# Performance work log

Hardware: AMD Instinct MI355X
Metric: run time of the kernel (lower is better)

The kernel has to match this reference:

```python
import jax, jax.numpy as jnp
import numpy as np

H = 8
D = 64  # head_dim = node_dim // num_heads = 512 // 8
NODE = 512
EPS = 1e-5


def setup_inputs() -> dict:
    key = jax.random.key(0)
    ks = jax.random.split(key, 8)
    S, IN = 4096, 1024
    return {
        "protT5_emb": jax.random.normal(ks[0], (S, IN), jnp.float32),
        "contact_matrix": jax.random.uniform(ks[1], (S, S), jnp.float32),
        "Wq": jax.random.normal(ks[2], (NODE, IN), jnp.float32) * 0.02,
        "bq": jnp.zeros((NODE,), jnp.float32),
        "Wk": jax.random.normal(ks[3], (NODE, IN), jnp.float32) * 0.02,
        "bk": jnp.zeros((NODE,), jnp.float32),
        "Wv": jax.random.normal(ks[4], (NODE, IN), jnp.float32) * 0.02,
        "bv": jnp.zeros((NODE,), jnp.float32),
        "Wc": jnp.ones((1, H, 1, 1), jnp.float32),
        "Wo": jax.random.normal(ks[5], (NODE, NODE), jnp.float32) * 0.02,
        "bo": jnp.zeros((NODE,), jnp.float32),
        "gamma": jnp.ones((NODE,), jnp.float32),
        "beta": jnp.zeros((NODE,), jnp.float32),
    }


def reference(protT5_emb, contact_matrix, Wq, bq, Wk, bk, Wv, bv, Wc, Wo, bo, gamma, beta):
    S = protT5_emb.shape[0]
    # QKV projections -> [H, S, D]
    Q = (protT5_emb @ Wq.T + bq).reshape(S, H, D).transpose(1, 0, 2)
    K = (protT5_emb @ Wk.T + bk).reshape(S, H, D).transpose(1, 0, 2)
    V = (protT5_emb @ Wv.T + bv).reshape(S, H, D).transpose(1, 0, 2)
    # raw scores [H, S, S]
    attn_raw = jnp.einsum('hsd,htd->hst', Q, K) / jnp.sqrt(jnp.float32(D))
    # multiplicative contact mask, per-head learnable scale
    contact_mask = contact_matrix[None, :, :] * Wc.reshape(H, 1, 1)
    attn_weight = jax.nn.softmax(attn_raw * contact_mask, axis=-1)
    attn_output = jnp.einsum('hst,htd->hsd', attn_weight, V)  # [H, S, D]
    # FAITHFUL to torch: transpose(0,1).view(S,-1) on [1,H,S,D] flattens in
    # (head, seq, dim) order -> scrambled [S, H*D] reshape, not head concat.
    attn_output = attn_output.reshape(S, H * D)
    aug = attn_output @ Wo.T + bo
    x = aug + protT5_emb[:, :NODE]
    mu = jnp.mean(x, axis=-1, keepdims=True)
    var = jnp.mean((x - mu) ** 2, axis=-1, keepdims=True)
    return (x - mu) * jax.lax.rsqrt(var + EPS) * gamma + beta
```

## Files before the change

kernel.cpp:

```cpp
#include <hip/hip_runtime.h>
#include <stdint.h>

#define SEQ 4096
#define INDIM 1024
#define NODEDIM 512
#define NH 8
#define HD 64
#define LSTR 72

typedef __bf16 bf16x8 __attribute__((ext_vector_type(8)));
typedef float f32x4 __attribute__((ext_vector_type(4)));

#define GLOAD_LDS(gp, lp) \
    __builtin_amdgcn_global_load_lds( \
        (const __attribute__((address_space(1))) void*)(gp), \
        (__attribute__((address_space(3))) void*)(lp), 16, 0, 0)

__device__ __forceinline__ unsigned short f2bf(float f) {
    union { float f; uint32_t u; } v; v.f = f;
    uint32_t u = v.u;
    uint32_t r = (u + 0x7fffu + ((u >> 16) & 1u)) >> 16;
    return (unsigned short)r;
}

__device__ __forceinline__ float fast_exp2(float x) {
    float r;
    asm volatile("v_exp_f32 %0, %1" : "=v"(r) : "v"(x));
    return r;
}

__global__ __launch_bounds__(256) void cvt_all(const float* __restrict__ emb,
                                               const float* __restrict__ Wq,
                                               const float* __restrict__ Wk,
                                               const float* __restrict__ Wv,
                                               const float* __restrict__ Wo,
                                               unsigned short* __restrict__ demb,
                                               unsigned short* __restrict__ dwqkv,
                                               unsigned short* __restrict__ dwo) {
    int b = blockIdx.x;
    const float* src;
    unsigned short* dst;
    int off;
    if (b < 4096)      { src = emb; dst = demb;            off = b; }
    else if (b < 4608) { src = Wq;  dst = dwqkv;           off = b - 4096; }
    else if (b < 5120) { src = Wk;  dst = dwqkv + 524288;  off = b - 4608; }
    else if (b < 5632) { src = Wv;  dst = dwqkv + 1048576; off = b - 5120; }
    else               { src = Wo;  dst = dwo;             off = b - 5632; }
    int i = (off * 256 + threadIdx.x) * 4;
    float4 v = *(const float4*)(src + i);
    ushort4 o;
    o.x = f2bf(v.x); o.y = f2bf(v.y); o.z = f2bf(v.z); o.w = f2bf(v.w);
    *(ushort4*)(dst + i) = o;
}

__global__ __launch_bounds__(256) void qkv_gemm(const unsigned short* __restrict__ A,
                                                const unsigned short* __restrict__ B,
                                                const float* __restrict__ bq,
                                                const float* __restrict__ bk,
                                                const float* __restrict__ bv,
                                                unsigned short* __restrict__ Qo,
                                                unsigned short* __restrict__ Ko,
                                                unsigned short* __restrict__ VTo) {
    __shared__ unsigned short As[128 * 32];
    __shared__ unsigned short Bs[128 * 32];
    __shared__ unsigned short Ts[128 * 40];
    const int tid = threadIdx.x;
    const int lane = tid & 63, wave = tid >> 6;
    const int wm = wave >> 1, wn = wave & 1;
    const int quad = lane >> 4, l16 = lane & 15;
    const int m0 = blockIdx.x * 128;
    const int n0 = blockIdx.y * 128;

    const int srow = tid >> 2, sqq = tid & 3;

    f32x4 acc[4][4] = {};

    for (int k0 = 0; k0 < INDIM; k0 += 32) {
        __syncthreads();
        for (int i = 0; i < 2; ++i) {
            int row = srow + 64 * i;
            GLOAD_LDS(A + (size_t)(m0 + row) * INDIM + k0 + sqq * 8, &As[row * 32 + sqq * 8]);
            GLOAD_LDS(B + (size_t)(n0 + row) * INDIM + k0 + sqq * 8, &Bs[row * 32 + sqq * 8]);
        }
        __syncthreads();
        bf16x8 af[4], bf[4];
        for (int mi = 0; mi < 4; ++mi)
            af[mi] = *(const bf16x8*)&As[(wm * 64 + mi * 16 + l16) * 32 + quad * 8];
        for (int ni = 0; ni < 4; ++ni)
            bf[ni] = *(const bf16x8*)&Bs[(wn * 64 + ni * 16 + l16) * 32 + quad * 8];
        for (int mi = 0; mi < 4; ++mi)
            for (int ni = 0; ni < 4; ++ni)
                acc[mi][ni] = __builtin_amdgcn_mfma_f32_16x16x32_bf16(af[mi], bf[ni], acc[mi][ni], 0, 0, 0);
    }

    if (blockIdx.y < 8) {
        unsigned short* outp = (blockIdx.y < 4) ? Qo : Ko;
        const float* biasp = (blockIdx.y < 4) ? bq : bk;
        for (int mi = 0; mi < 4; ++mi)
            for (int ni = 0; ni < 4; ++ni)
                for (int r = 0; r < 4; ++r) {
                    int s = m0 + wm * 64 + mi * 16 + quad * 4 + r;
                    int n = n0 + wn * 64 + ni * 16 + l16;
                    int h = (n >> 6) & 7;
                    int dd = n & 63;
                    float v = acc[mi][ni][r] + biasp[n & 511];
                    outp[((size_t)h * SEQ + s) * HD + dd] = f2bf(v);
                }
    } else {
        for (int chunk = 0; chunk < 4; ++chunk) {
            const int cwm = chunk >> 1;
            const int milo = (chunk & 1) * 2;
            __syncthreads();
            if (wm == cwm) {
                for (int mi2 = 0; mi2 < 2; ++mi2) {
                    int mi = milo + mi2;
                    for (int ni = 0; ni < 4; ++ni) {
                        int ddf = wn * 64 + ni * 16 + l16;
                        float bias = bv[(n0 + ddf) & 511];
                        for (int r = 0; r < 4; ++r) {
                            int sl = mi2 * 16 + quad * 4 + r;
                            Ts[ddf * 40 + sl] = f2bf(acc[mi][ni][r] + bias);
                        }
                    }
                }
            }
            __syncthreads();
            for (int pass = 0; pass < 2; ++pass) {
                int c = pass * 256 + tid;
                int row = c >> 2, part = c & 3;
                int nfull = n0 + row;
                int h = (nfull >> 6) & 7, dd = nfull & 63;
                *(bf16x8*)(VTo + ((size_t)h * HD + dd) * SEQ + m0 + chunk * 32 + part * 8) =
                    *(const bf16x8*)&Ts[row * 40 + part * 8];
            }
        }
    }
}

__global__ __launch_bounds__(256, 3) void attn_kernel(const unsigned short* __restrict__ Q,
                                                      const unsigned short* __restrict__ K,
                                                      const unsigned short* __restrict__ VT,
                                                      const float* __restrict__ CM,
                                                      const float* __restrict__ Wc,
                                                      float* __restrict__ O0,
                                                      float* __restrict__ O1,
                                                      float* __restrict__ O2,
                                                      float* __restrict__ O3,
                                                      float* __restrict__ l0,
                                                      float* __restrict__ l1,
                                                      float* __restrict__ l2,
                                                      float* __restrict__ l3,
                                                      int nsplit) {
    __shared__ unsigned short QPs[128 * LSTR];
    __shared__ unsigned short Ks[64 * LSTR];
    __shared__ unsigned short Vs[64 * LSTR];
    const int tid = threadIdx.x;
    const int lane = tid & 63, wave = tid >> 6;
    const int quad = lane >> 4, l16 = lane & 15;
    const int h = blockIdx.y;
    const int q0 = blockIdx.x * 128;
    const int split = blockIdx.z;
    float* __restrict__ Op = (split == 0) ? O0 : (split == 1) ? O1 : (split == 2) ? O2 : O3;
    float* __restrict__ lp = (split == 0) ? l0 : (split == 1) ? l1 : (split == 2) ? l2 : l3;
    const float wch = Wc[h] * 0.125f * 1.44269504f;

    const int qt = 64 / nsplit, rt = 64 % nsplit;
    const int tb_tiles = split * qt + (split < rt ? split : rt);
    const int ntiles = qt + (split < rt ? 1 : 0);
    const int tbeg = tb_tiles * 64;
    const int tend = tbeg + ntiles * 64;

    for (int i = 0; i < 4; ++i) {
        int c = tid + 256 * i;
        int row = c >> 3, part = c & 7;
        bf16x8 v = *(const bf16x8*)(Q + ((size_t)h * SEQ + q0 + row) * HD + part * 8);
        for (int j = 0; j < 8; ++j) v[j] = (__bf16)((float)v[j] * wch);
        *(bf16x8*)&QPs[row * LSTR + part * 8] = v;
    }

    const int srow0 = tid >> 3, spart = tid & 7;
    const int srow1 = (tid + 256) >> 3;
    const unsigned short* kp0 = K + ((size_t)h * SEQ + tbeg + srow0) * HD + spart * 8;
    const unsigned short* kp1 = K + ((size_t)h * SEQ + tbeg + srow1) * HD + spart * 8;
    const unsigned short* vp0 = VT + ((size_t)h * HD + srow0) * SEQ + tbeg + spart * 8;
    const unsigned short* vp1 = VT + ((size_t)h * HD + srow1) * SEQ + tbeg + spart * 8;
    bf16x8 kr0 = *(const bf16x8*)kp0;
    bf16x8 kr1 = *(const bf16x8*)kp1;
    bf16x8 vr0 = *(const bf16x8*)vp0;
    bf16x8 vr1 = *(const bf16x8*)vp1;

    __syncthreads();
    bf16x8 a[2][2];
    for (int mi = 0; mi < 2; ++mi) {
        a[mi][0] = *(const bf16x8*)&QPs[(wave * 32 + mi * 16 + l16) * LSTR + quad * 8];
        a[mi][1] = *(const bf16x8*)&QPs[(wave * 32 + mi * 16 + l16) * LSTR + 32 + quad * 8];
    }

    f32x4 O[2][4] = {};
    float l_part[2][4] = {};
    const float* cmbase0 = CM + (size_t)(q0 + wave * 32 + quad * 4) * SEQ + l16;
    const float* cmbase1 = cmbase0 + (size_t)16 * SEQ;
    const int sw = (l16 >> 2) & 3;

    for (int t0 = tbeg; t0 < tend; t0 += 64) {
        float cmv[2][4][4];
        for (int r = 0; r < 4; ++r)
            for (int nt = 0; nt < 4; ++nt) {
                cmv[0][r][nt] = cmbase0[(size_t)r * SEQ + t0 + nt * 16];
                cmv[1][r][nt] = cmbase1[(size_t)r * SEQ + t0 + nt * 16];
            }

        __syncthreads();
        *(bf16x8*)&Ks[srow0 * LSTR + spart * 8] = kr0;
        *(bf16x8*)&Ks[srow1 * LSTR + spart * 8] = kr1;
        *(bf16x8*)&Vs[srow0 * LSTR + spart * 8] = vr0;
        *(bf16x8*)&Vs[srow1 * LSTR + spart * 8] = vr1;
        __syncthreads();

        if (t0 + 64 < tend) {
            kr0 = *(const bf16x8*)(kp0 + (size_t)(t0 + 64 - tbeg) * HD);
            kr1 = *(const bf16x8*)(kp1 + (size_t)(t0 + 64 - tbeg) * HD);
            vr0 = *(const bf16x8*)(vp0 + (t0 + 64 - tbeg));
            vr1 = *(const bf16x8*)(vp1 + (t0 + 64 - tbeg));
        }

        f32x4 sc[2][4];
        for (int nt = 0; nt < 4; ++nt) {
            bf16x8 b0 = *(const bf16x8*)&Ks[(nt * 16 + l16) * LSTR + quad * 8];
            bf16x8 b1 = *(const bf16x8*)&Ks[(nt * 16 + l16) * LSTR + 32 + quad * 8];
            for (int mi = 0; mi < 2; ++mi) {
                f32x4 z = {0.f, 0.f, 0.f, 0.f};
                z = __builtin_amdgcn_mfma_f32_16x16x32_bf16(a[mi][0], b0, z, 0, 0, 0);
                z = __builtin_amdgcn_mfma_f32_16x16x32_bf16(a[mi][1], b1, z, 0, 0, 0);
                sc[mi][nt] = z;
            }
        }

        for (int mi = 0; mi < 2; ++mi)
            for (int r = 0; r < 4; ++r)
                for (int nt = 0; nt < 4; ++nt) {
                    float pv = fast_exp2(sc[mi][nt][r] * cmv[mi][r][nt]);
                    l_part[mi][r] += pv;
                    union { float f; uint32_t u; } pu; pu.f = pv;
                    QPs[(wave * 32 + mi * 16 + quad * 4 + r) * LSTR
                        + (((nt * 2 + (l16 >> 3)) ^ quad) << 3) + (l16 & 7)] =
                        (unsigned short)(pu.u >> 16);
                }

        asm volatile("s_waitcnt lgkmcnt(0)" ::: "memory");

        bf16x8 pa[2][2];
        for (int mi = 0; mi < 2; ++mi) {
            pa[mi][0] = *(const bf16x8*)&QPs[(wave * 32 + mi * 16 + l16) * LSTR + ((quad ^ sw) << 3)];
            pa[mi][1] = *(const bf16x8*)&QPs[(wave * 32 + mi * 16 + l16) * LSTR + 32 + ((quad ^ sw) << 3)];
        }
        for (int nt = 0; nt < 4; ++nt) {
            bf16x8 vb0 = *(const bf16x8*)&Vs[(nt * 16 + l16) * LSTR + quad * 8];
            bf16x8 vb1 = *(const bf16x8*)&Vs[(nt * 16 + l16) * LSTR + 32 + quad * 8];
            for (int mi = 0; mi < 2; ++mi) {
                f32x4 o = O[mi][nt];
                o = __builtin_amdgcn_mfma_f32_16x16x32_bf16(pa[mi][0], vb0, o, 0, 0, 0);
                o = __builtin_amdgcn_mfma_f32_16x16x32_bf16(pa[mi][1], vb1, o, 0, 0, 0);
                O[mi][nt] = o;
            }
        }
    }

    for (int mi = 0; mi < 2; ++mi)
        for (int r = 0; r < 4; ++r) {
            float s = l_part[mi][r];
            for (int off = 1; off < 16; off <<= 1) s += __shfl_xor(s, off);
            l_part[mi][r] = s;
        }
    if (l16 == 0)
        for (int mi = 0; mi < 2; ++mi)
            for (int r = 0; r < 4; ++r)
                lp[(size_t)h * SEQ + q0 + wave * 32 + mi * 16 + quad * 4 + r] = l_part[mi][r];
    for (int mi = 0; mi < 2; ++mi)
        for (int nt = 0; nt < 4; ++nt)
            for (int r = 0; r < 4; ++r) {
                int sg = q0 + wave * 32 + mi * 16 + quad * 4 + r;
                Op[((size_t)h * SEQ + sg) * HD + nt * 16 + l16] = O[mi][nt][r];
            }
}

__global__ __launch_bounds__(256) void combine_kernel(const float* __restrict__ O0,
                                                      const float* __restrict__ O1,
                                                      const float* __restrict__ O2,
                                                      const float* __restrict__ O3,
                                                      const float* __restrict__ l0,
                                                      const float* __restrict__ l1,
                                                      const float* __restrict__ l2,
                                                      const float* __restrict__ l3,
                                                      int nsplit,
                                                      unsigned short* __restrict__ AO) {
    int idx = blockIdx.x * 256 + threadIdx.x;
    int e = idx * 4;
    int row = e >> 6;
    float4 a = *(const float4*)(O0 + e);
    float4 b = *(const float4*)(O1 + e);
    float x = a.x + b.x, y = a.y + b.y, z = a.z + b.z, w = a.w + b.w;
    float ls = l0[row] + l1[row];
    if (nsplit >= 3) {
        float4 c = *(const float4*)(O2 + e);
        x += c.x; y += c.y; z += c.z; w += c.w;
        ls += l2[row];
    }
    if (nsplit >= 4) {
        float4 d = *(const float4*)(O3 + e);
        x += d.x; y += d.y; z += d.z; w += d.w;
        ls += l3[row];
    }
    float linv = 1.f / ls;
    ushort4 o;
    o.x = f2bf(x * linv);
    o.y = f2bf(y * linv);
    o.z = f2bf(z * linv);
    o.w = f2bf(w * linv);
    *(ushort4*)(AO + e) = o;
}

__global__ __launch_bounds__(256) void out_gemm(const unsigned short* __restrict__ A,
                                                const unsigned short* __restrict__ B,
                                                const float* __restrict__ bo,
                                                const float* __restrict__ emb,
                                                float* __restrict__ X) {
    __shared__ unsigned short As[64 * 32];
    __shared__ unsigned short Bs[128 * 32];
    const int tid = threadIdx.x;
    const int lane = tid & 63, wave = tid >> 6;
    const int quad = lane >> 4, l16 = lane & 15;
    const int m0 = blockIdx.x * 64;
    const int n0 = blockIdx.y * 128;

    const int srow = tid >> 2, sqq = tid & 3;

    f32x4 acc[8] = {};

    for (int k0 = 0; k0 < NODEDIM; k0 += 32) {
        __syncthreads();
        GLOAD_LDS(A + (size_t)(m0 + srow) * NODEDIM + k0 + sqq * 8, &As[srow * 32 + sqq * 8]);
        for (int i = 0; i < 2; ++i) {
            int row = srow + 64 * i;
            GLOAD_LDS(B + (size_t)(n0 + row) * NODEDIM + k0 + sqq * 8, &Bs[row * 32 + sqq * 8]);
        }
        __syncthreads();
        bf16x8 af = *(const bf16x8*)&As[(wave * 16 + l16) * 32 + quad * 8];
        for (int ni = 0; ni < 8; ++ni) {
            bf16x8 bf = *(const bf16x8*)&Bs[(ni * 16 + l16) * 32 + quad * 8];
            acc[ni] = __builtin_amdgcn_mfma_f32_16x16x32_bf16(af, bf, acc[ni], 0, 0, 0);
        }
    }

    for (int ni = 0; ni < 8; ++ni)
        for (int r = 0; r < 4; ++r) {
            int s = m0 + wave * 16 + quad * 4 + r;
            int n = n0 + ni * 16 + l16;
            float v = acc[ni][r] + bo[n] + emb[(size_t)s * INDIM + n];
            X[(size_t)s * NODEDIM + n] = v;
        }
}

__global__ __launch_bounds__(256) void ln_kernel(const float* __restrict__ X,
                                                 const float* __restrict__ gamma,
                                                 const float* __restrict__ beta,
                                                 float* __restrict__ out) {
    const int s = blockIdx.x;
    const int n = threadIdx.x * 2;
    float2 v = *(const float2*)&X[(size_t)s * NODEDIM + n];
    float sum = v.x + v.y;
    float sq = v.x * v.x + v.y * v.y;
    for (int off = 32; off > 0; off >>= 1) {
        sum += __shfl_down(sum, off);
        sq += __shfl_down(sq, off);
    }
    __shared__ float ssum[4], ssq[4];
    const int wave = threadIdx.x >> 6, lane = threadIdx.x & 63;
    if (lane == 0) { ssum[wave] = sum; ssq[wave] = sq; }
    __syncthreads();
    float tsum = ssum[0] + ssum[1] + ssum[2] + ssum[3];
    float tsq = ssq[0] + ssq[1] + ssq[2] + ssq[3];
    float mu = tsum * (1.f / 512.f);
    float var = tsq * (1.f / 512.f) - mu * mu;
    float rstd = rsqrtf(var + 1e-5f);
    float2 g = *(const float2*)&gamma[n];
    float2 b = *(const float2*)&beta[n];
    float2 o;
    o.x = (v.x - mu) * rstd * g.x + b.x;
    o.y = (v.y - mu) * rstd * g.y + b.y;
    *(float2*)&out[(size_t)s * NODEDIM + n] = o;
}

extern "C" void kernel_launch(void* const* d_in, const int* in_sizes, int n_in,
                              void* d_out, int out_size, void* d_ws, size_t ws_size,
                              hipStream_t stream) {
    const float* emb = (const float*)d_in[0];
    const float* cm  = (const float*)d_in[1];
    const float* Wq  = (const float*)d_in[2];
    const float* bq  = (const float*)d_in[3];
    const float* Wk  = (const float*)d_in[4];
    const float* bk  = (const float*)d_in[5];
    const float* Wv  = (const float*)d_in[6];
    const float* bv  = (const float*)d_in[7];
    const float* Wc  = (const float*)d_in[8];
    const float* Wo  = (const float*)d_in[9];
    const float* bo  = (const float*)d_in[10];
    const float* gamma = (const float*)d_in[11];
    const float* beta  = (const float*)d_in[12];
    float* out = (float*)d_out;

    unsigned short* ws = (unsigned short*)d_ws;
    unsigned short* emb_bf  = ws;
    unsigned short* wqkv_bf = emb_bf + 4194304;
    unsigned short* wo_bf   = wqkv_bf + 1572864;
    unsigned short* Qb  = wo_bf + 262144;
    unsigned short* Kb  = Qb + 2097152;
    unsigned short* VTb = Kb + 2097152;
    unsigned short* AOb = VTb + 2097152;
    float* X = (float*)(AOb + 2097152);
    float* O0 = (float*)emb_bf;
    float* O1 = X;
    float* O2 = X + 2097152;
    float* O3 = O2 + 2097152;
    float* l0 = (float*)wqkv_bf;
    float* l1 = l0 + NH * SEQ;
    float* l2 = l1 + NH * SEQ;
    float* l3 = l2 + NH * SEQ;

    const size_t NEED3 = 45613056ull;
    const int nz = (ws_size >= NEED3) ? 3 : 2;

    cvt_all<<<5888, 256, 0, stream>>>(emb, Wq, Wk, Wv, Wo, emb_bf, wqkv_bf, wo_bf);

    qkv_gemm<<<dim3(32, 12), 256, 0, stream>>>(emb_bf, wqkv_bf, bq, bk, bv, Qb, Kb, VTb);
    attn_kernel<<<dim3(32, 8, nz), 256, 0, stream>>>(Qb, Kb, VTb, cm, Wc,
                                                     O0, O1, O2, O3, l0, l1, l2, l3, nz);
    combine_kernel<<<2048, 256, 0, stream>>>(O0, O1, O2, O3, l0, l1, l2, l3, nz, AOb);
    out_gemm<<<dim3(64, 4), 256, 0, stream>>>(AOb, wo_bf, bo, emb, X);
    ln_kernel<<<4096, 256, 0, stream>>>(X, gamma, beta, out);
}
```

Before: 250.1 us.

## Process two heads per attention block to reuse contact-matrix loads

Each attention block now handles two heads, so every contact-matrix tile read from global memory serves both heads. This halves the heavy fp32 contact-matrix traffic, which is the dominant memory stream. To keep the grid filled, the key dimension is split four ways instead of three when workspace allows, and the occupancy hint drops from 3 to 2 blocks per CU. The cost is higher register and LDS use per block, and the 4-way split assumes SEQ divides evenly by nsplit.

```diff
diff --git a/kernel.cpp b/kernel.cpp
--- a/kernel.cpp
+++ b/kernel.cpp
@@ -137,7 +137,7 @@
     }
 }
 
-__global__ __launch_bounds__(256, 3) void attn_kernel(const unsigned short* __restrict__ Q,
+__global__ __launch_bounds__(256, 2) void attn_kernel(const unsigned short* __restrict__ Q,
                                                       const unsigned short* __restrict__ K,
                                                       const unsigned short* __restrict__ VT,
                                                       const float* __restrict__ CM,
@@ -152,52 +152,68 @@
                                                       float* __restrict__ l3,
                                                       int nsplit) {
     __shared__ unsigned short QPs[128 * LSTR];
-    __shared__ unsigned short Ks[64 * LSTR];
-    __shared__ unsigned short Vs[64 * LSTR];
+    __shared__ unsigned short Ks[2][64 * LSTR];
+    __shared__ unsigned short Vs[2][64 * LSTR];
     const int tid = threadIdx.x;
     const int lane = tid & 63, wave = tid >> 6;
     const int quad = lane >> 4, l16 = lane & 15;
-    const int h = blockIdx.y;
+    const int h0 = blockIdx.y * 2, h1 = h0 + 1;
     const int q0 = blockIdx.x * 128;
     const int split = blockIdx.z;
     float* __restrict__ Op = (split == 0) ? O0 : (split == 1) ? O1 : (split == 2) ? O2 : O3;
     float* __restrict__ lp = (split == 0) ? l0 : (split == 1) ? l1 : (split == 2) ? l2 : l3;
-    const float wch = Wc[h] * 0.125f * 1.44269504f;
-
-    const int qt = 64 / nsplit, rt = 64 % nsplit;
-    const int tb_tiles = split * qt + (split < rt ? split : rt);
-    const int ntiles = qt + (split < rt ? 1 : 0);
-    const int tbeg = tb_tiles * 64;
-    const int tend = tbeg + ntiles * 64;
-
+    const float wch0 = Wc[h0] * 0.125f * 1.44269504f;
+    const float wch1 = Wc[h1] * 0.125f * 1.44269504f;
+
+    const int tcount = SEQ / nsplit;
+    const int tbeg = split * tcount;
+    const int tend = tbeg + tcount;
+
+    bf16x8 a0[2][2], a1[2][2];
     for (int i = 0; i < 4; ++i) {
         int c = tid + 256 * i;
         int row = c >> 3, part = c & 7;
-        bf16x8 v = *(const bf16x8*)(Q + ((size_t)h * SEQ + q0 + row) * HD + part * 8);
-        for (int j = 0; j < 8; ++j) v[j] = (__bf16)((float)v[j] * wch);
+        bf16x8 v = *(const bf16x8*)(Q + ((size_t)h0 * SEQ + q0 + row) * HD + part * 8);
+        for (int j = 0; j < 8; ++j) v[j] = (__bf16)((float)v[j] * wch0);
         *(bf16x8*)&QPs[row * LSTR + part * 8] = v;
+    }
+    __syncthreads();
+    for (int mi = 0; mi < 2; ++mi) {
+        a0[mi][0] = *(const bf16x8*)&QPs[(wave * 32 + mi * 16 + l16) * LSTR + quad * 8];
+        a0[mi][1] = *(const bf16x8*)&QPs[(wave * 32 + mi * 16 + l16) * LSTR + 32 + quad * 8];
+    }
+    __syncthreads();
+    for (int i = 0; i < 4; ++i) {
+        int c = tid + 256 * i;
+        int row = c >> 3, part = c & 7;
+        bf16x8 v = *(const bf16x8*)(Q + ((size_t)h1 * SEQ + q0 + row) * HD + part * 8);
+        for (int j = 0; j < 8; ++j) v[j] = (__bf16)((float)v[j] * wch1);
+        *(bf16x8*)&QPs[row * LSTR + part * 8] = v;
+    }
+    __syncthreads();
+    for (int mi = 0; mi < 2; ++mi) {
+        a1[mi][0] = *(const bf16x8*)&QPs[(wave * 32 + mi * 16 + l16) * LSTR + quad * 8];
+        a1[mi][1] = *(const bf16x8*)&QPs[(wave * 32 + mi * 16 + l16) * LSTR + 32 + quad * 8];
     }
 
     const int srow0 = tid >> 3, spart = tid & 7;
     const int srow1 = (tid + 256) >> 3;
-    const unsigned short* kp0 = K + ((size_t)h * SEQ + tbeg + srow0) * HD + spart * 8;
-    const unsigned short* kp1 = K + ((size_t)h * SEQ + tbeg + srow1) * HD + spart * 8;
-    const unsigned short* vp0 = VT + ((size_t)h * HD + srow0) * SEQ + tbeg + spart * 8;
-    const unsigned short* vp1 = VT + ((size_t)h * HD + srow1) * SEQ + tbeg + spart * 8;
-    bf16x8 kr0 = *(const bf16x8*)kp0;
-    bf16x8 kr1 = *(const bf16x8*)kp1;
-    bf16x8 vr0 = *(const bf16x8*)vp0;
-    bf16x8 vr1 = *(const bf16x8*)vp1;
-
-    __syncthreads();
-    bf16x8 a[2][2];
-    for (int mi = 0; mi < 2; ++mi) {
-        a[mi][0] = *(const bf16x8*)&QPs[(wave * 32 + mi * 16 + l16) * LSTR + quad * 8];
-        a[mi][1] = *(const bf16x8*)&QPs[(wave * 32 + mi * 16 + l16) * LSTR + 32 + quad * 8];
-    }
-
-    f32x4 O[2][4] = {};
-    float l_part[2][4] = {};
+    const size_t hoff = (size_t)SEQ * HD;
+    const unsigned short* kp0 = K + ((size_t)h0 * SEQ + tbeg + srow0) * HD + spart * 8;
+    const unsigned short* kp1 = K + ((size_t)h0 * SEQ + tbeg + srow1) * HD + spart * 8;
+    const unsigned short* vp0 = VT + ((size_t)h0 * HD + srow0) * SEQ + tbeg + spart * 8;
+    const unsigned short* vp1 = VT + ((size_t)h0 * HD + srow1) * SEQ + tbeg + spart * 8;
+    bf16x8 kr0a = *(const bf16x8*)kp0;
+    bf16x8 kr1a = *(const bf16x8*)kp1;
+    bf16x8 vr0a = *(const bf16x8*)vp0;
+    bf16x8 vr1a = *(const bf16x8*)vp1;
+    bf16x8 kr0b = *(const bf16x8*)(kp0 + hoff);
+    bf16x8 kr1b = *(const bf16x8*)(kp1 + hoff);
+    bf16x8 vr0b = *(const bf16x8*)(vp0 + hoff);
+    bf16x8 vr1b = *(const bf16x8*)(vp1 + hoff);
+
+    f32x4 Oa[2][4] = {}, Ob[2][4] = {};
+    float l_pa[2][4] = {}, l_pb[2][4] = {};
     const float* cmbase0 = CM + (size_t)(q0 + wave * 32 + quad * 4) * SEQ + l16;
     const float* cmbase1 = cmbase0 + (size_t)16 * SEQ;
     const int sw = (l16 >> 2) & 3;
@@ -211,76 +227,130 @@
             }
 
         __syncthreads();
-        *(bf16x8*)&Ks[srow0 * LSTR + spart * 8] = kr0;
-        *(bf16x8*)&Ks[srow1 * LSTR + spart * 8] = kr1;
-        *(bf16x8*)&Vs[srow0 * LSTR + spart * 8] = vr0;
-        *(bf16x8*)&Vs[srow1 * LSTR + spart * 8] = vr1;
+        *(bf16x8*)&Ks[0][srow0 * LSTR + spart * 8] = kr0a;
+        *(bf16x8*)&Ks[0][srow1 * LSTR + spart * 8] = kr1a;
+        *(bf16x8*)&Vs[0][srow0 * LSTR + spart * 8] = vr0a;
+        *(bf16x8*)&Vs[0][srow1 * LSTR + spart * 8] = vr1a;
+        *(bf16x8*)&Ks[1][srow0 * LSTR + spart * 8] = kr0b;
+        *(bf16x8*)&Ks[1][srow1 * LSTR + spart * 8] = kr1b;
+        *(bf16x8*)&Vs[1][srow0 * LSTR + spart * 8] = vr0b;
+        *(bf16x8*)&Vs[1][srow1 * LSTR + spart * 8] = vr1b;
         __syncthreads();
 
         if (t0 + 64 < tend) {
-            kr0 = *(const bf16x8*)(kp0 + (size_t)(t0 + 64 - tbeg) * HD);
-            kr1 = *(const bf16x8*)(kp1 + (size_t)(t0 + 64 - tbeg) * HD);
-            vr0 = *(const bf16x8*)(vp0 + (t0 + 64 - tbeg));
-            vr1 = *(const bf16x8*)(vp1 + (t0 + 64 - tbeg));
-        }
-
-        f32x4 sc[2][4];
-        for (int nt = 0; nt < 4; ++nt) {
-            bf16x8 b0 = *(const bf16x8*)&Ks[(nt * 16 + l16) * LSTR + quad * 8];
-            bf16x8 b1 = *(const bf16x8*)&Ks[(nt * 16 + l16) * LSTR + 32 + quad * 8];
+            int d = t0 + 64 - tbeg;
+            kr0a = *(const bf16x8*)(kp0 + (size_t)d * HD);
+            kr1a = *(const bf16x8*)(kp1 + (size_t)d * HD);
+            vr0a = *(const bf16x8*)(vp0 + d);
+            vr1a = *(const bf16x8*)(vp1 + d);
+            kr0b = *(const bf16x8*)(kp0 + (size_t)d * HD + hoff);
+            kr1b = *(const bf16x8*)(kp1 + (size_t)d * HD + hoff);
+            vr0b = *(const bf16x8*)(vp0 + d + hoff);
+            vr1b = *(const bf16x8*)(vp1 + d + hoff);
+        }
+
+        {
+            f32x4 sc[2][4];
+            for (int nt = 0; nt < 4; ++nt) {
+                bf16x8 b0 = *(const bf16x8*)&Ks[0][(nt * 16 + l16) * LSTR + quad * 8];
+                bf16x8 b1 = *(const bf16x8*)&Ks[0][(nt * 16 + l16) * LSTR + 32 + quad * 8];
+                for (int mi = 0; mi < 2; ++mi) {
+                    f32x4 z = {0.f, 0.f, 0.f, 0.f};
+                    z = __builtin_amdgcn_mfma_f32_16x16x32_bf16(a0[mi][0], b0, z, 0, 0, 0);
+                    z = __builtin_amdgcn_mfma_f32_16x16x32_bf16(a0[mi][1], b1, z, 0, 0, 0);
+                    sc[mi][nt] = z;
+                }
+            }
+            for (int mi = 0; mi < 2; ++mi)
+                for (int r = 0; r < 4; ++r)
+                    for (int nt = 0; nt < 4; ++nt) {
+                        float pv = fast_exp2(sc[mi][nt][r] * cmv[mi][r][nt]);
+                        l_pa[mi][r] += pv;
+                        union { float f; uint32_t u; } pu; pu.f = pv;
+                        QPs[(wave * 32 + mi * 16 + quad * 4 + r) * LSTR
+                            + (((nt * 2 + (l16 >> 3)) ^ quad) << 3) + (l16 & 7)] =
+                            (unsigned short)(pu.u >> 16);
+                    }
+            asm volatile("s_waitcnt lgkmcnt(0)" ::: "memory");
+            bf16x8 pa[2][2];
             for (int mi = 0; mi < 2; ++mi) {
-                f32x4 z = {0.f, 0.f, 0.f, 0.f};
-                z = __builtin_amdgcn_mfma_f32_16x16x32_bf16(a[mi][0], b0, z, 0, 0, 0);
-                z = __builtin_amdgcn_mfma_f32_16x16x32_bf16(a[mi][1], b1, z, 0, 0, 0);
-                sc[mi][nt] = z;
-            }
-        }
-
-        for (int mi = 0; mi < 2; ++mi)
-            for (int r = 0; r < 4; ++r)
-                for (int nt = 0; nt < 4; ++nt) {
-                    float pv = fast_exp2(sc[mi][nt][r] * cmv[mi][r][nt]);
-                    l_part[mi][r] += pv;
-                    union { float f; uint32_t u; } pu; pu.f = pv;
-                    QPs[(wave * 32 + mi * 16 + quad * 4 + r) * LSTR
-                        + (((nt * 2 + (l16 >> 3)) ^ quad) << 3) + (l16 & 7)] =
-                        (unsigned short)(pu.u >> 16);
+                pa[mi][0] = *(const bf16x8*)&QPs[(wave * 32 + mi * 16 + l16) * LSTR + ((quad ^ sw) << 3)];
+                pa[mi][1] = *(const bf16x8*)&QPs[(wave * 32 + mi * 16 + l16) * LSTR + 32 + ((quad ^ sw) << 3)];
+            }
+            for (int nt = 0; nt < 4; ++nt) {
+                bf16x8 vb0 = *(const bf16x8*)&Vs[0][(nt * 16 + l16) * LSTR + quad * 8];
+                bf16x8 vb1 = *(const bf16x8*)&Vs[0][(nt * 16 + l16) * LSTR + 32 + quad * 8];
+                for (int mi = 0; mi < 2; ++mi) {
+                    f32x4 o = Oa[mi][nt];
+                    o = __builtin_amdgcn_mfma_f32_16x16x32_bf16(pa[mi][0], vb0, o, 0, 0, 0);
+                    o = __builtin_amdgcn_mfma_f32_16x16x32_bf16(pa[mi][1], vb1, o, 0, 0, 0);
+                    Oa[mi][nt] = o;
                 }
-
-        asm volatile("s_waitcnt lgkmcnt(0)" ::: "memory");
-
-        bf16x8 pa[2][2];
-        for (int mi = 0; mi < 2; ++mi) {
-            pa[mi][0] = *(const bf16x8*)&QPs[(wave * 32 + mi * 16 + l16) * LSTR + ((quad ^ sw) << 3)];
-            pa[mi][1] = *(const bf16x8*)&QPs[(wave * 32 + mi * 16 + l16) * LSTR + 32 + ((quad ^ sw) << 3)];
-        }
-        for (int nt = 0; nt < 4; ++nt) {
-            bf16x8 vb0 = *(const bf16x8*)&Vs[(nt * 16 + l16) * LSTR + quad * 8];
-            bf16x8 vb1 = *(const bf16x8*)&Vs[(nt * 16 + l16) * LSTR + 32 + quad * 8];
+            }
+        }
+        {
+            f32x4 sc[2][4];
+            for (int nt = 0; nt < 4; ++nt) {
+                bf16x8 b0 = *(const bf16x8*)&Ks[1][(nt * 16 + l16) * LSTR + quad * 8];
+                bf16x8 b1 = *(const bf16x8*)&Ks[1][(nt * 16 + l16) * LSTR + 32 + quad * 8];
+                for (int mi = 0; mi < 2; ++mi) {
+                    f32x4 z = {0.f, 0.f, 0.f, 0.f};
+                    z = __builtin_amdgcn_mfma_f32_16x16x32_bf16(a1[mi][0], b0, z, 0, 0, 0);
+                    z = __builtin_amdgcn_mfma_f32_16x16x32_bf16(a1[mi][1], b1, z, 0, 0, 0);
+                    sc[mi][nt] = z;
+                }
+            }
+            for (int mi = 0; mi < 2; ++mi)
+                for (int r = 0; r < 4; ++r)
+                    for (int nt = 0; nt < 4; ++nt) {
+                        float pv = fast_exp2(sc[mi][nt][r] * cmv[mi][r][nt]);
+                        l_pb[mi][r] += pv;
+                        union { float f; uint32_t u; } pu; pu.f = pv;
+                        QPs[(wave * 32 + mi * 16 + quad * 4 + r) * LSTR
+                            + (((nt * 2 + (l16 >> 3)) ^ quad) << 3) + (l16 & 7)] =
+                            (unsigned short)(pu.u >> 16);
+                    }
+            asm volatile("s_waitcnt lgkmcnt(0)" ::: "memory");
+            bf16x8 pa[2][2];
             for (int mi = 0; mi < 2; ++mi) {
-                f32x4 o = O[mi][nt];
-                o = __builtin_amdgcn_mfma_f32_16x16x32_bf16(pa[mi][0], vb0, o, 0, 0, 0);
-                o = __builtin_amdgcn_mfma_f32_16x16x32_bf16(pa[mi][1], vb1, o, 0, 0, 0);
-                O[mi][nt] = o;
+                pa[mi][0] = *(const bf16x8*)&QPs[(wave * 32 + mi * 16 + l16) * LSTR + ((quad ^ sw) << 3)];
+                pa[mi][1] = *(const bf16x8*)&QPs[(wave * 32 + mi * 16 + l16) * LSTR + 32 + ((quad ^ sw) << 3)];
+            }
+            for (int nt = 0; nt < 4; ++nt) {
+                bf16x8 vb0 = *(const bf16x8*)&Vs[1][(nt * 16 + l16) * LSTR + quad * 8];
+                bf16x8 vb1 = *(const bf16x8*)&Vs[1][(nt * 16 + l16) * LSTR + 32 + quad * 8];
+                for (int mi = 0; mi < 2; ++mi) {
+                    f32x4 o = Ob[mi][nt];
+                    o = __builtin_amdgcn_mfma_f32_16x16x32_bf16(pa[mi][0], vb0, o, 0, 0, 0);
+                    o = __builtin_amdgcn_mfma_f32_16x16x32_bf16(pa[mi][1], vb1, o, 0, 0, 0);
+                    Ob[mi][nt] = o;
+                }
             }
         }
     }
 
     for (int mi = 0; mi < 2; ++mi)
         for (int r = 0; r < 4; ++r) {
-            float s = l_part[mi][r];
+            float s = l_pa[mi][r];
             for (int off = 1; off < 16; off <<= 1) s += __shfl_xor(s, off);
-            l_part[mi][r] = s;
+            l_pa[mi][r] = s;
+            float s2 = l_pb[mi][r];
+            for (int off = 1; off < 16; off <<= 1) s2 += __shfl_xor(s2, off);
+            l_pb[mi][r] = s2;
         }
     if (l16 == 0)
         for (int mi = 0; mi < 2; ++mi)
-            for (int r = 0; r < 4; ++r)
-                lp[(size_t)h * SEQ + q0 + wave * 32 + mi * 16 + quad * 4 + r] = l_part[mi][r];
+            for (int r = 0; r < 4; ++r) {
+                int sg = q0 + wave * 32 + mi * 16 + quad * 4 + r;
+                lp[(size_t)h0 * SEQ + sg] = l_pa[mi][r];
+                lp[(size_t)h1 * SEQ + sg] = l_pb[mi][r];
+            }
     for (int mi = 0; mi < 2; ++mi)
         for (int nt = 0; nt < 4; ++nt)
             for (int r = 0; r < 4; ++r) {
                 int sg = q0 + wave * 32 + mi * 16 + quad * 4 + r;
-                Op[((size_t)h * SEQ + sg) * HD + nt * 16 + l16] = O[mi][nt][r];
+                Op[((size_t)h0 * SEQ + sg) * HD + nt * 16 + l16] = Oa[mi][nt][r];
+                Op[((size_t)h1 * SEQ + sg) * HD + nt * 16 + l16] = Ob[mi][nt][r];
             }
 }
 
@@ -427,13 +497,13 @@
     float* l2 = l1 + NH * SEQ;
     float* l3 = l2 + NH * SEQ;
 
-    const size_t NEED3 = 45613056ull;
-    const int nz = (ws_size >= NEED3) ? 3 : 2;
+    const size_t NEED4 = 54001664ull;
+    const int nz = (ws_size >= NEED4) ? 4 : 2;
 
     cvt_all<<<5888, 256, 0, stream>>>(emb, Wq, Wk, Wv, Wo, emb_bf, wqkv_bf, wo_bf);
 
     qkv_gemm<<<dim3(32, 12), 256, 0, stream>>>(emb_bf, wqkv_bf, bq, bk, bv, Qb, Kb, VTb);
-    attn_kernel<<<dim3(32, 8, nz), 256, 0, stream>>>(Qb, Kb, VTb, cm, Wc,
+    attn_kernel<<<dim3(32, 4, nz), 256, 0, stream>>>(Qb, Kb, VTb, cm, Wc,
                                                      O0, O1, O2, O3, l0, l1, l2, l3, nz);
     combine_kernel<<<2048, 256, 0, stream>>>(O0, O1, O2, O3, l0, l1, l2, l3, nz, AOb);
     out_gemm<<<dim3(64, 4), 256, 0, stream>>>(AOb, wo_bf, bo, emb, X);
```

Result: no change. 252.0 us (+0.8%).

## Transpose QK^T MFMA, vectorize contact-mask loads, read V directly from global

Applied to the files above, without the earlier changes.

Swaps the MFMA operand order for the score computation so each lane holds four consecutive key columns of one query row. The contact matrix can then be read as float4 per lane, the bf16 probabilities written to LDS as packed 64-bit stores, and the row-sum reduced with only two shuffles. V is no longer staged in LDS: each lane loads its V^T fragments straight from global memory every tile. This drops one LDS buffer and its stores, and trades fewer, wider CM loads and LDS writes for uncoalesced or redundant global V reads.

```diff
diff --git a/kernel.cpp b/kernel.cpp
--- a/kernel.cpp
+++ b/kernel.cpp
@@ -153,7 +153,6 @@
                                                       int nsplit) {
     __shared__ unsigned short QPs[128 * LSTR];
     __shared__ unsigned short Ks[64 * LSTR];
-    __shared__ unsigned short Vs[64 * LSTR];
     const int tid = threadIdx.x;
     const int lane = tid & 63, wave = tid >> 6;
     const int quad = lane >> 4, l16 = lane & 15;
@@ -182,12 +181,8 @@
     const int srow1 = (tid + 256) >> 3;
     const unsigned short* kp0 = K + ((size_t)h * SEQ + tbeg + srow0) * HD + spart * 8;
     const unsigned short* kp1 = K + ((size_t)h * SEQ + tbeg + srow1) * HD + spart * 8;
-    const unsigned short* vp0 = VT + ((size_t)h * HD + srow0) * SEQ + tbeg + spart * 8;
-    const unsigned short* vp1 = VT + ((size_t)h * HD + srow1) * SEQ + tbeg + spart * 8;
     bf16x8 kr0 = *(const bf16x8*)kp0;
     bf16x8 kr1 = *(const bf16x8*)kp1;
-    bf16x8 vr0 = *(const bf16x8*)vp0;
-    bf16x8 vr1 = *(const bf16x8*)vp1;
 
     __syncthreads();
     bf16x8 a[2][2];
@@ -197,55 +192,59 @@
     }
 
     f32x4 O[2][4] = {};
-    float l_part[2][4] = {};
-    const float* cmbase0 = CM + (size_t)(q0 + wave * 32 + quad * 4) * SEQ + l16;
-    const float* cmbase1 = cmbase0 + (size_t)16 * SEQ;
+    float l_lane[2] = {0.f, 0.f};
     const int sw = (l16 >> 2) & 3;
+    const unsigned short* vtb = VT + ((size_t)h * HD + l16) * SEQ;
 
     for (int t0 = tbeg; t0 < tend; t0 += 64) {
-        float cmv[2][4][4];
-        for (int r = 0; r < 4; ++r)
-            for (int nt = 0; nt < 4; ++nt) {
-                cmv[0][r][nt] = cmbase0[(size_t)r * SEQ + t0 + nt * 16];
-                cmv[1][r][nt] = cmbase1[(size_t)r * SEQ + t0 + nt * 16];
-            }
+        bf16x8 vb[4][2];
+        for (int nt = 0; nt < 4; ++nt) {
+            vb[nt][0] = *(const bf16x8*)(vtb + (size_t)(nt * 16) * SEQ + t0 + quad * 8);
+            vb[nt][1] = *(const bf16x8*)(vtb + (size_t)(nt * 16) * SEQ + t0 + 32 + quad * 8);
+        }
 
         __syncthreads();
         *(bf16x8*)&Ks[srow0 * LSTR + spart * 8] = kr0;
         *(bf16x8*)&Ks[srow1 * LSTR + spart * 8] = kr1;
-        *(bf16x8*)&Vs[srow0 * LSTR + spart * 8] = vr0;
-        *(bf16x8*)&Vs[srow1 * LSTR + spart * 8] = vr1;
         __syncthreads();
 
         if (t0 + 64 < tend) {
             kr0 = *(const bf16x8*)(kp0 + (size_t)(t0 + 64 - tbeg) * HD);
             kr1 = *(const bf16x8*)(kp1 + (size_t)(t0 + 64 - tbeg) * HD);
-            vr0 = *(const bf16x8*)(vp0 + (t0 + 64 - tbeg));
-            vr1 = *(const bf16x8*)(vp1 + (t0 + 64 - tbeg));
-        }
-
-        f32x4 sc[2][4];
-        for (int nt = 0; nt < 4; ++nt) {
-            bf16x8 b0 = *(const bf16x8*)&Ks[(nt * 16 + l16) * LSTR + quad * 8];
-            bf16x8 b1 = *(const bf16x8*)&Ks[(nt * 16 + l16) * LSTR + 32 + quad * 8];
-            for (int mi = 0; mi < 2; ++mi) {
+        }
+
+        for (int mi = 0; mi < 2; ++mi) {
+            const float* cmb = CM + (size_t)(q0 + wave * 32 + mi * 16 + l16) * SEQ + t0 + quad * 4;
+            float4 cm4[4];
+            for (int nt = 0; nt < 4; ++nt)
+                cm4[nt] = *(const float4*)(cmb + nt * 16);
+            f32x4 sc[4];
+            for (int nt = 0; nt < 4; ++nt) {
+                bf16x8 k0 = *(const bf16x8*)&Ks[(nt * 16 + l16) * LSTR + quad * 8];
+                bf16x8 k1 = *(const bf16x8*)&Ks[(nt * 16 + l16) * LSTR + 32 + quad * 8];
                 f32x4 z = {0.f, 0.f, 0.f, 0.f};
-                z = __builtin_amdgcn_mfma_f32_16x16x32_bf16(a[mi][0], b0, z, 0, 0, 0);
-                z = __builtin_amdgcn_mfma_f32_16x16x32_bf16(a[mi][1], b1, z, 0, 0, 0);
-                sc[mi][nt] = z;
-            }
-        }
-
-        for (int mi = 0; mi < 2; ++mi)
-            for (int r = 0; r < 4; ++r)
-                for (int nt = 0; nt < 4; ++nt) {
-                    float pv = fast_exp2(sc[mi][nt][r] * cmv[mi][r][nt]);
-                    l_part[mi][r] += pv;
-                    union { float f; uint32_t u; } pu; pu.f = pv;
-                    QPs[(wave * 32 + mi * 16 + quad * 4 + r) * LSTR
-                        + (((nt * 2 + (l16 >> 3)) ^ quad) << 3) + (l16 & 7)] =
-                        (unsigned short)(pu.u >> 16);
-                }
+                z = __builtin_amdgcn_mfma_f32_16x16x32_bf16(k0, a[mi][0], z, 0, 0, 0);
+                z = __builtin_amdgcn_mfma_f32_16x16x32_bf16(k1, a[mi][1], z, 0, 0, 0);
+                sc[nt] = z;
+            }
+            float ll = 0.f;
+            for (int nt = 0; nt < 4; ++nt) {
+                float p0 = fast_exp2(sc[nt][0] * cm4[nt].x);
+                float p1 = fast_exp2(sc[nt][1] * cm4[nt].y);
+                float p2 = fast_exp2(sc[nt][2] * cm4[nt].z);
+                float p3 = fast_exp2(sc[nt][3] * cm4[nt].w);
+                ll += (p0 + p1) + (p2 + p3);
+                union { float f; uint32_t u; } u0, u1, u2, u3;
+                u0.f = p0; u1.f = p1; u2.f = p2; u3.f = p3;
+                uint32_t w0 = (u0.u >> 16) | (u1.u & 0xFFFF0000u);
+                uint32_t w1 = (u2.u >> 16) | (u3.u & 0xFFFF0000u);
+                unsigned long long w = (unsigned long long)w0 | ((unsigned long long)w1 << 32);
+                int chunk = (2 * nt + (quad >> 1)) ^ sw;
+                *(unsigned long long*)&QPs[(wave * 32 + mi * 16 + l16) * LSTR
+                                           + (chunk << 3) + ((quad & 1) << 2)] = w;
+            }
+            l_lane[mi] += ll;
+        }
 
         asm volatile("s_waitcnt lgkmcnt(0)" ::: "memory");
 
@@ -254,28 +253,22 @@
             pa[mi][0] = *(const bf16x8*)&QPs[(wave * 32 + mi * 16 + l16) * LSTR + ((quad ^ sw) << 3)];
             pa[mi][1] = *(const bf16x8*)&QPs[(wave * 32 + mi * 16 + l16) * LSTR + 32 + ((quad ^ sw) << 3)];
         }
-        for (int nt = 0; nt < 4; ++nt) {
-            bf16x8 vb0 = *(const bf16x8*)&Vs[(nt * 16 + l16) * LSTR + quad * 8];
-            bf16x8 vb1 = *(const bf16x8*)&Vs[(nt * 16 + l16) * LSTR + 32 + quad * 8];
+        for (int nt = 0; nt < 4; ++nt)
             for (int mi = 0; mi < 2; ++mi) {
                 f32x4 o = O[mi][nt];
-                o = __builtin_amdgcn_mfma_f32_16x16x32_bf16(pa[mi][0], vb0, o, 0, 0, 0);
-                o = __builtin_amdgcn_mfma_f32_16x16x32_bf16(pa[mi][1], vb1, o, 0, 0, 0);
+                o = __builtin_amdgcn_mfma_f32_16x16x32_bf16(pa[mi][0], vb[nt][0], o, 0, 0, 0);
+                o = __builtin_amdgcn_mfma_f32_16x16x32_bf16(pa[mi][1], vb[nt][1], o, 0, 0, 0);
                 O[mi][nt] = o;
             }
-        }
-    }
-
-    for (int mi = 0; mi < 2; ++mi)
-        for (int r = 0; r < 4; ++r) {
-            float s = l_part[mi][r];
-            for (int off = 1; off < 16; off <<= 1) s += __shfl_xor(s, off);
-            l_part[mi][r] = s;
-        }
-    if (l16 == 0)
-        for (int mi = 0; mi < 2; ++mi)
-            for (int r = 0; r < 4; ++r)
-                lp[(size_t)h * SEQ + q0 + wave * 32 + mi * 16 + quad * 4 + r] = l_part[mi][r];
+    }
+
+    for (int mi = 0; mi < 2; ++mi) {
+        float s = l_lane[mi];
+        s += __shfl_xor(s, 16);
+        s += __shfl_xor(s, 32);
+        if (quad == 0)
+            lp[(size_t)h * SEQ + q0 + wave * 32 + mi * 16 + l16] = s;
+    }
     for (int mi = 0; mi < 2; ++mi)
         for (int nt = 0; nt < 4; ++nt)
             for (int r = 0; r < 4; ++r) {
```

Measured after the change: 344.0 us. 37.6% more time.
